# Optimization experiments

Measured on AMD Instinct MI355X. Metric: run time of the kernel, lower is better.

Reference implementation:

```python
import jax, jax.numpy as jnp
import numpy as np

N, E = 50000, 800000
IN_DIM = 128
OUT_DIM = 128
H = 8
D = OUT_DIM // H  # head_dim = 16
LN_EPS = 1e-5


def setup_inputs() -> dict:
    key = jax.random.key(0)
    ks = jax.random.split(key, 16)
    s_in = 1.0 / np.sqrt(IN_DIM)
    s_out = 1.0 / np.sqrt(OUT_DIM)
    return {
        "x": jax.random.normal(ks[0], (N, IN_DIM), dtype=jnp.float32),
        "edge_index": jax.random.randint(ks[1], (2, E), 0, N, dtype=jnp.int32),
        "edge_attr": jax.random.uniform(ks[2], (E,), dtype=jnp.float32),
        # per-head TransformerConv params, stacked over heads (heads=1 per conv)
        "Wq": jax.random.normal(ks[3], (H, IN_DIM, D), dtype=jnp.float32) * s_in,
        "bq": jnp.zeros((H, D), dtype=jnp.float32),
        "Wk": jax.random.normal(ks[4], (H, IN_DIM, D), dtype=jnp.float32) * s_in,
        "bk": jnp.zeros((H, D), dtype=jnp.float32),
        "Wv": jax.random.normal(ks[5], (H, IN_DIM, D), dtype=jnp.float32) * s_in,
        "bv": jnp.zeros((H, D), dtype=jnp.float32),
        "We": jax.random.normal(ks[6], (H, D), dtype=jnp.float32),  # lin_edge (edge_dim=1, no bias)
        "Wskip": jax.random.normal(ks[7], (H, IN_DIM, D), dtype=jnp.float32) * s_in,
        "bskip": jnp.zeros((H, D), dtype=jnp.float32),
        "Wo": jax.random.normal(ks[8], (OUT_DIM, OUT_DIM), dtype=jnp.float32) * s_out,
        "bo": jnp.zeros((OUT_DIM,), dtype=jnp.float32),
        "gamma": jnp.ones((OUT_DIM,), dtype=jnp.float32),
        "beta": jnp.zeros((OUT_DIM,), dtype=jnp.float32),
    }


def reference(x, edge_index, edge_attr, Wq, bq, Wk, bk, Wv, bv, We, Wskip, bskip, Wo, bo, gamma, beta):
    n = x.shape[0]
    h, _, d = Wq.shape
    src, dst = edge_index[0], edge_index[1]
    # node-level projections for all heads at once: [N, H, D]
    q = jnp.einsum('ni,hid->nhd', x, Wq) + bq
    k = jnp.einsum('ni,hid->nhd', x, Wk) + bk
    v = jnp.einsum('ni,hid->nhd', x, Wv) + bv
    # edge embedding: lin_edge on scalar edge_attr -> [E, H, D]
    e = edge_attr[:, None, None] * We[None, :, :]
    # attention logits per edge/head: q_dst . (k_src + e) / sqrt(d)
    ke = k[src] + e
    alpha = jnp.einsum('ehd,ehd->eh', q[dst], ke) / jnp.sqrt(jnp.asarray(d, x.dtype))
    # segment softmax over destination nodes
    m = jax.ops.segment_max(alpha, dst, num_segments=n)  # [N, H]
    m = jnp.where(jnp.isfinite(m), m, 0.0)
    ex = jnp.exp(alpha - m[dst])
    denom = jax.ops.segment_sum(ex, dst, num_segments=n)
    w = ex / jnp.maximum(denom[dst], 1e-16)  # [E, H]
    # weighted aggregation of (v_src + e)
    agg = jax.ops.segment_sum(w[:, :, None] * (v[src] + e), dst, num_segments=n)  # [N, H, D]
    # root/skip connection inside each TransformerConv
    skip = jnp.einsum('ni,hid->nhd', x, Wskip) + bskip
    heads_cat = (agg + skip).reshape(n, h * d)  # concat over heads -> [N, OUT_DIM]
    out = heads_cat @ Wo + bo
    out = out + x  # residual (in_dim == out_dim)
    mu = out.mean(-1, keepdims=True)
    var = out.var(-1, keepdims=True)
    out = (out - mu) * jax.lax.rsqrt(var + LN_EPS) * gamma + beta
    return out
```

## Files before the change

kernel.cpp:

```cpp
#include <hip/hip_runtime.h>
#include <hip/hip_bf16.h>
#include <stdint.h>
#include <math.h>

#define IN_DIM 128
#define H_HEADS 8
#define HD 16

typedef __attribute__((ext_vector_type(8))) short bf16x8;
typedef __attribute__((ext_vector_type(4))) float f32x4;

__device__ __forceinline__ unsigned short f2bf(float f) {
    __hip_bfloat16 h = __float2bfloat16(f);
    return reinterpret_cast<unsigned short&>(h);
}
__device__ __forceinline__ float bf2f(unsigned short h) {
    return __uint_as_float(((unsigned int)h) << 16);
}

__device__ __forceinline__ void split_f8(const float4 f0, const float4 f1,
                                         bf16x8& h8, bf16x8& l8) {
    float ff[8] = {f0.x, f0.y, f0.z, f0.w, f1.x, f1.y, f1.z, f1.w};
    union { bf16x8 v; unsigned short u[8]; } H, L;
#pragma unroll
    for (int j = 0; j < 8; ++j) {
        H.u[j] = f2bf(ff[j]);
        L.u[j] = f2bf(ff[j] - bf2f(H.u[j]));
    }
    h8 = H.v; l8 = L.v;
}

__device__ __forceinline__ void stage_B(const unsigned short* __restrict__ src,
                                        unsigned short* __restrict__ lds, int t)
{
#pragma unroll
    for (int j = 0; j < 8; ++j) {
        int idx16 = t + j * 256;
        int c = idx16 >> 4, kcol = idx16 & 15;
        uint4 v = *reinterpret_cast<const uint4*>(src + (size_t)c * 128 + kcol * 8);
        *reinterpret_cast<uint4*>(lds + c * 128 + ((kcol ^ (c & 15)) * 8)) = v;
    }
}
__device__ __forceinline__ bf16x8 read_B(const unsigned short* __restrict__ lds,
                                         int c, int kcol)
{
    return *reinterpret_cast<const bf16x8*>(lds + c * 128 + ((kcol ^ (c & 15)) * 8));
}

__global__ __launch_bounds__(256)
void prep_count_kernel(const float* __restrict__ Wq, const float* __restrict__ Wk,
                       const float* __restrict__ Wv, const float* __restrict__ Wsk,
                       const float* __restrict__ Wo,
                       const float* __restrict__ bq, const float* __restrict__ bk,
                       const float* __restrict__ bv, const float* __restrict__ bsk,
                       unsigned short* __restrict__ WtH, unsigned short* __restrict__ WtL,
                       float* __restrict__ bias_cat,
                       const int* __restrict__ ei, int* __restrict__ deg, int E)
{
    const int b = blockIdx.x;
    const int t = threadIdx.x;
    if (b >= 5) {
        int e = (b - 5) * 256 + t;
        if (e < E) atomicAdd(&deg[ei[E + e]], 1);
        return;
    }
    const int p = b;
    const float* src = (p == 0) ? Wq : (p == 1) ? Wk : (p == 2) ? Wv : (p == 3) ? Wsk : Wo;
    unsigned short* dh = WtH + (size_t)p * 16384;
    unsigned short* dl = WtL + (size_t)p * 16384;
#pragma unroll
    for (int j = 0; j < 64; ++j) {
        int o = t + j * 256;
        int c = o >> 7, k = o & 127;
        float v;
        if (p < 4) {
            int h = c >> 4, d = c & 15;
            v = src[(size_t)h * 2048 + (size_t)k * 16 + d];
        } else {
            v = src[(size_t)k * 128 + c];
        }
        unsigned short hi = f2bf(v);
        unsigned short lo = f2bf(v - bf2f(hi));
        dh[o] = hi; dl[o] = lo;
    }
    if (p < 4 && t < 128) {
        const float* bb = (p == 0) ? bq : (p == 1) ? bk : (p == 2) ? bv : bsk;
        bias_cat[p * 128 + t] = bb[t];
    }
}

__global__ __launch_bounds__(256)
void gemm_proj_kernel(const float* __restrict__ A,
                      const unsigned short* __restrict__ WtH_base,
                      const unsigned short* __restrict__ WtL_base,
                      const float* __restrict__ bias_cat,
                      float* __restrict__ qout, float* __restrict__ skipout,
                      unsigned short* __restrict__ kvout, int N)
{
    __shared__ unsigned short Bs[16384];
    const int t = threadIdx.x;
    const int lane = t & 63;
    const int w = t >> 6;
    const int lr = lane & 15;
    const int lk = lane >> 4;
    const int pr = blockIdx.y;
    const int brow0 = blockIdx.x * 64 + w * 16;
    const int arow = min(brow0 + lr, N - 1);
    const float* ap = A + (size_t)arow * 128;

    bf16x8 ah[4], al[4];
#pragma unroll
    for (int ks = 0; ks < 4; ++ks) {
        float4 f0 = *reinterpret_cast<const float4*>(ap + ks * 32 + lk * 8);
        float4 f1 = *reinterpret_cast<const float4*>(ap + ks * 32 + lk * 8 + 4);
        split_f8(f0, f1, ah[ks], al[ks]);
    }

    for (int pp = 0; pp < 2; ++pp) {
        const int p = pr * 2 + pp;
        f32x4 acc[8];
#pragma unroll
        for (int ni = 0; ni < 8; ++ni) acc[ni] = (f32x4){0.f, 0.f, 0.f, 0.f};

        __syncthreads();
        stage_B(WtH_base + (size_t)p * 16384, Bs, t);
        __syncthreads();
#pragma unroll
        for (int ks = 0; ks < 4; ++ks)
#pragma unroll
            for (int ni = 0; ni < 8; ++ni) {
                bf16x8 bh = read_B(Bs, ni * 16 + lr, ks * 4 + lk);
                acc[ni] = __builtin_amdgcn_mfma_f32_16x16x32_bf16(ah[ks], bh, acc[ni], 0, 0, 0);
                acc[ni] = __builtin_amdgcn_mfma_f32_16x16x32_bf16(al[ks], bh, acc[ni], 0, 0, 0);
            }
        __syncthreads();
        stage_B(WtL_base + (size_t)p * 16384, Bs, t);
        __syncthreads();
#pragma unroll
        for (int ks = 0; ks < 4; ++ks)
#pragma unroll
            for (int ni = 0; ni < 8; ++ni) {
                bf16x8 bl = read_B(Bs, ni * 16 + lr, ks * 4 + lk);
                acc[ni] = __builtin_amdgcn_mfma_f32_16x16x32_bf16(ah[ks], bl, acc[ni], 0, 0, 0);
            }

        const float* bias = bias_cat + p * 128;
        if (p == 0 || p == 3) {
            float* outp = (p == 0) ? qout : skipout;
#pragma unroll
            for (int ni = 0; ni < 8; ++ni) {
                int col = ni * 16 + lr;
                float bc = bias[col];
#pragma unroll
                for (int r = 0; r < 4; ++r) {
                    int gr = brow0 + lk * 4 + r;
                    if (gr < N) outp[(size_t)gr * 128 + col] = acc[ni][r] + bc;
                }
            }
        } else {
            unsigned int* kvu = (unsigned int*)kvout;
            const int slot = (p == 1) ? 0 : 1;
#pragma unroll
            for (int ni = 0; ni < 8; ++ni) {
                int col = ni * 16 + lr;
                float bc = bias[col];
#pragma unroll
                for (int r = 0; r < 4; ++r) {
                    unsigned int s = f2bf(acc[ni][r] + bc);
                    unsigned int o = __shfl_xor((int)s, 1);
                    int gr = brow0 + lk * 4 + r;
                    if (((lr & 1) == 0) && gr < N)
                        kvu[(size_t)gr * 128 + 2 * (col >> 1) + slot] = s | (o << 16);
                }
            }
        }
    }
}

__global__ __launch_bounds__(256)
void gemm_out_ln_kernel(const float* __restrict__ A,
                        const unsigned short* __restrict__ BtH_t,
                        const unsigned short* __restrict__ BtL_t,
                        const float* __restrict__ bo,
                        const float* __restrict__ res,
                        const float* __restrict__ gamma,
                        const float* __restrict__ beta,
                        float* __restrict__ out, int N)
{
    __shared__ unsigned short Bs[16384];
    const int t = threadIdx.x;
    const int lane = t & 63;
    const int w = t >> 6;
    const int lr = lane & 15;
    const int lk = lane >> 4;
    const int brow0 = blockIdx.x * 64 + w * 16;
    const int arow = min(brow0 + lr, N - 1);
    const float* ap = A + (size_t)arow * 128;

    bf16x8 ah[4], al[4];
#pragma unroll
    for (int ks = 0; ks < 4; ++ks) {
        float4 f0 = *reinterpret_cast<const float4*>(ap + ks * 32 + lk * 8);
        float4 f1 = *reinterpret_cast<const float4*>(ap + ks * 32 + lk * 8 + 4);
        split_f8(f0, f1, ah[ks], al[ks]);
    }

    f32x4 acc[8];
#pragma unroll
    for (int ni = 0; ni < 8; ++ni) acc[ni] = (f32x4){0.f, 0.f, 0.f, 0.f};

    stage_B(BtH_t, Bs, t);
    __syncthreads();
#pragma unroll
    for (int ks = 0; ks < 4; ++ks)
#pragma unroll
        for (int ni = 0; ni < 8; ++ni) {
            bf16x8 bh = read_B(Bs, ni * 16 + lr, ks * 4 + lk);
            acc[ni] = __builtin_amdgcn_mfma_f32_16x16x32_bf16(ah[ks], bh, acc[ni], 0, 0, 0);
            acc[ni] = __builtin_amdgcn_mfma_f32_16x16x32_bf16(al[ks], bh, acc[ni], 0, 0, 0);
        }
    __syncthreads();
    stage_B(BtL_t, Bs, t);
    __syncthreads();
#pragma unroll
    for (int ks = 0; ks < 4; ++ks)
#pragma unroll
        for (int ni = 0; ni < 8; ++ni) {
            bf16x8 bl = read_B(Bs, ni * 16 + lr, ks * 4 + lk);
            acc[ni] = __builtin_amdgcn_mfma_f32_16x16x32_bf16(ah[ks], bl, acc[ni], 0, 0, 0);
        }

#pragma unroll
    for (int ni = 0; ni < 8; ++ni) {
        int col = ni * 16 + lr;
        float bc = bo[col];
#pragma unroll
        for (int r = 0; r < 4; ++r) {
            int gr = brow0 + lk * 4 + r;
            float rv = (gr < N) ? res[(size_t)gr * 128 + col] : 0.f;
            acc[ni][r] += bc + rv;
        }
    }
#pragma unroll
    for (int r = 0; r < 4; ++r) {
        float s = 0.f, sq = 0.f;
#pragma unroll
        for (int ni = 0; ni < 8; ++ni) { float v = acc[ni][r]; s += v; sq += v * v; }
#pragma unroll
        for (int mk = 1; mk < 16; mk <<= 1) {
            s  += __shfl_xor(s, mk);
            sq += __shfl_xor(sq, mk);
        }
        float mean = s * (1.0f / 128.0f);
        float var  = sq * (1.0f / 128.0f) - mean * mean;
        float inv  = rsqrtf(var + 1e-5f);
        int gr = brow0 + lk * 4 + r;
        if (gr < N) {
#pragma unroll
            for (int ni = 0; ni < 8; ++ni) {
                int col = ni * 16 + lr;
                out[(size_t)gr * 128 + col] =
                    (acc[ni][r] - mean) * inv * gamma[col] + beta[col];
            }
        }
    }
}

__global__ __launch_bounds__(1024)
void scan_part1(const int* __restrict__ deg, int* __restrict__ offs,
                int* __restrict__ csums, int N)
{
    __shared__ int wsum[16];
    const int t = threadIdx.x;
    const int lane = t & 63, wid = t >> 6;
    const int idx = blockIdx.x * 4096 + t * 4;
    int v[4];
#pragma unroll
    for (int j = 0; j < 4; ++j) { int i = idx + j; v[j] = (i < N) ? deg[i] : 0; }
    int ls = v[0] + v[1] + v[2] + v[3];
    int inc = ls;
#pragma unroll
    for (int off = 1; off < 64; off <<= 1) {
        int y = __shfl_up(inc, off);
        if (lane >= off) inc += y;
    }
    if (lane == 63) wsum[wid] = inc;
    __syncthreads();
    if (t < 16) {
        int winc = wsum[t];
        for (int off = 1; off < 16; off <<= 1) {
            int y = __shfl_up(winc, off);
            if (t >= off) winc += y;
        }
        wsum[t] = winc;
    }
    __syncthreads();
    int wexcl = (wid == 0) ? 0 : wsum[wid - 1];
    int texcl = wexcl + (inc - ls);
    int pre = 0;
#pragma unroll
    for (int j = 0; j < 4; ++j) {
        int i = idx + j;
        if (i < N) offs[i] = texcl + pre;
        pre += v[j];
    }
    if (t == 0) csums[blockIdx.x] = wsum[15];
}

__global__ void scan_part2(int* __restrict__ csums, int nc,
                           int* __restrict__ offs, int N)
{
    const int t = threadIdx.x;
    int v = (t < nc) ? csums[t] : 0;
    int inc = v;
#pragma unroll
    for (int off = 1; off < 64; off <<= 1) {
        int y = __shfl_up(inc, off);
        if (t >= off) inc += y;
    }
    if (t < nc) csums[t] = inc - v;
    int total = __shfl(inc, nc - 1);
    if (t == 0) offs[N] = total;
}

__global__ __launch_bounds__(1024)
void scan_part3(int* __restrict__ offs, const int* __restrict__ csums,
                int* __restrict__ cursor, int N)
{
    const int coff = csums[blockIdx.x];
    const int idx = blockIdx.x * 4096 + threadIdx.x * 4;
#pragma unroll
    for (int j = 0; j < 4; ++j) {
        int i = idx + j;
        if (i < N) { int val = offs[i] + coff; offs[i] = val; cursor[i] = val; }
    }
}

__global__ void scatter_kernel(const int* __restrict__ ei, const float* __restrict__ ea,
                               int* __restrict__ cursor, int2* __restrict__ csr, int E)
{
    int e = blockIdx.x * 256 + threadIdx.x;
    if (e < E) {
        int s = ei[e], d = ei[E + e];
        int pos = atomicAdd(&cursor[d], 1);
        csr[pos] = make_int2(s, __float_as_int(ea[e]));
    }
}

__global__ __launch_bounds__(256)
void agg_kernel(const float* __restrict__ qb, const float* __restrict__ sb,
                const unsigned short* __restrict__ kvb,
                const int* __restrict__ offs, const int2* __restrict__ csr,
                const float* __restrict__ We, float* __restrict__ heads_cat, int N)
{
    const int lane = threadIdx.x & 63;
    const int node = blockIdx.x * 4 + (threadIdx.x >> 6);
    if (node >= N) return;
    const int q16  = lane & 15;
    const int quad = lane >> 4;

    const float4 qa = *reinterpret_cast<const float4*>(qb + (size_t)node * 128 + 8 * q16);
    const float4 qc = *reinterpret_cast<const float4*>(qb + (size_t)node * 128 + 8 * q16 + 4);
    const float4 wa = *reinterpret_cast<const float4*>(We + 8 * q16);
    const float4 wc = *reinterpret_cast<const float4*>(We + 8 * q16 + 4);

    float qwe = qa.x * wa.x + qa.y * wa.y + qa.z * wa.z + qa.w * wa.w
              + qc.x * wc.x + qc.y * wc.y + qc.z * wc.z + qc.w * wc.w;
    qwe += __shfl_xor(qwe, 1);

    const int e0 = offs[node];
    const int cnt = offs[node + 1] - e0;
    const int myCnt = (cnt > quad) ? ((cnt - quad + 3) >> 2) : 0;
    const int2* cp = csr + e0 + quad;
    const unsigned int* kvu = (const unsigned int*)kvb;

    float m = -__builtin_huge_valf();
    float s = 0.f, sWE = 0.f;
    float a0 = 0.f, a1 = 0.f, a2 = 0.f, a3 = 0.f;
    float a4 = 0.f, a5 = 0.f, a6 = 0.f, a7 = 0.f;

#define KVG(ec, ga, gb) do { \
    const uint4* p_ = reinterpret_cast<const uint4*>(kvu + (size_t)(ec).x * 128 + 8 * q16); \
    ga = p_[0]; gb = p_[1]; } while (0)

    int2 c0, c1, c2;
    uint4 g0a, g0b, g1a, g1b;
    if (myCnt > 0) c0 = cp[0];
    if (myCnt > 1) c1 = cp[4];
    if (myCnt > 2) c2 = cp[8];
    if (myCnt > 0) KVG(c0, g0a, g0b);
    if (myCnt > 1) KVG(c1, g1a, g1b);

    for (int j = 0; j < myCnt; ++j) {
        const float eav = __int_as_float(c0.y);
        float k0 = __uint_as_float(g0a.x << 16);
        float k1 = __uint_as_float(g0a.x & 0xffff0000u);
        float k2 = __uint_as_float(g0a.z << 16);
        float k3 = __uint_as_float(g0a.z & 0xffff0000u);
        float k4 = __uint_as_float(g0b.x << 16);
        float k5 = __uint_as_float(g0b.x & 0xffff0000u);
        float k6 = __uint_as_float(g0b.z << 16);
        float k7 = __uint_as_float(g0b.z & 0xffff0000u);
        float part = qa.x * k0 + qa.y * k1 + qa.z * k2 + qa.w * k3
                   + qc.x * k4 + qc.y * k5 + qc.z * k6 + qc.w * k7;
        part += __shfl_xor(part, 1);
        float alpha = fmaf(eav, qwe, part) * 0.25f;
        float d = alpha - m;
        if (__any(d > 8.f)) {
            float nm = fmaxf(m, alpha);
            float sc = __expf(m - nm);
            m = nm; d = alpha - m;
            s *= sc; sWE *= sc;
            a0 *= sc; a1 *= sc; a2 *= sc; a3 *= sc;
            a4 *= sc; a5 *= sc; a6 *= sc; a7 *= sc;
        }
        float pv = __expf(d);
        s += pv;
        sWE = fmaf(pv, eav, sWE);
        float v0 = __uint_as_float(g0a.y << 16);
        float v1 = __uint_as_float(g0a.y & 0xffff0000u);
        float v2 = __uint_as_float(g0a.w << 16);
        float v3 = __uint_as_float(g0a.w & 0xffff0000u);
        float v4 = __uint_as_float(g0b.y << 16);
        float v5 = __uint_as_float(g0b.y & 0xffff0000u);
        float v6 = __uint_as_float(g0b.w << 16);
        float v7 = __uint_as_float(g0b.w & 0xffff0000u);
        a0 = fmaf(pv, v0, a0); a1 = fmaf(pv, v1, a1);
        a2 = fmaf(pv, v2, a2); a3 = fmaf(pv, v3, a3);
        a4 = fmaf(pv, v4, a4); a5 = fmaf(pv, v5, a5);
        a6 = fmaf(pv, v6, a6); a7 = fmaf(pv, v7, a7);
        c0 = c1; c1 = c2;
        g0a = g1a; g0b = g1b;
        if (j + 3 < myCnt) c2 = cp[4 * j + 12];
        if (j + 2 < myCnt) KVG(c1, g1a, g1b);
    }

#pragma unroll
    for (int mk = 16; mk <= 32; mk <<= 1) {
        float om  = __shfl_xor(m, mk);
        float os  = __shfl_xor(s, mk);
        float oWE = __shfl_xor(sWE, mk);
        float o0 = __shfl_xor(a0, mk), o1 = __shfl_xor(a1, mk);
        float o2 = __shfl_xor(a2, mk), o3 = __shfl_xor(a3, mk);
        float o4 = __shfl_xor(a4, mk), o5 = __shfl_xor(a5, mk);
        float o6 = __shfl_xor(a6, mk), o7 = __shfl_xor(a7, mk);
        float nm = fmaxf(m, om);
        float eS = (s  > 0.f) ? __expf(m  - nm) : 0.f;
        float eO = (os > 0.f) ? __expf(om - nm) : 0.f;
        m = nm;
        s   = s  * eS + os  * eO;
        sWE = sWE * eS + oWE * eO;
        a0 = a0 * eS + o0 * eO; a1 = a1 * eS + o1 * eO;
        a2 = a2 * eS + o2 * eO; a3 = a3 * eS + o3 * eO;
        a4 = a4 * eS + o4 * eO; a5 = a5 * eS + o5 * eO;
        a6 = a6 * eS + o6 * eO; a7 = a7 * eS + o7 * eO;
    }

    if (quad == 0) {
        float inv = 1.0f / fmaxf(s, 1e-16f);
        const float4 s0 = *reinterpret_cast<const float4*>(sb + (size_t)node * 128 + 8 * q16);
        const float4 s1 = *reinterpret_cast<const float4*>(sb + (size_t)node * 128 + 8 * q16 + 4);
        float4 oA, oB;
        oA.x = fmaf(sWE, wa.x, a0) * inv + s0.x;
        oA.y = fmaf(sWE, wa.y, a1) * inv + s0.y;
        oA.z = fmaf(sWE, wa.z, a2) * inv + s0.z;
        oA.w = fmaf(sWE, wa.w, a3) * inv + s0.w;
        oB.x = fmaf(sWE, wc.x, a4) * inv + s1.x;
        oB.y = fmaf(sWE, wc.y, a5) * inv + s1.y;
        oB.z = fmaf(sWE, wc.z, a6) * inv + s1.z;
        oB.w = fmaf(sWE, wc.w, a7) * inv + s1.w;
        *reinterpret_cast<float4*>(heads_cat + (size_t)node * 128 + 8 * q16)     = oA;
        *reinterpret_cast<float4*>(heads_cat + (size_t)node * 128 + 8 * q16 + 4) = oB;
    }
#undef KVG
}

extern "C" void kernel_launch(void* const* d_in, const int* in_sizes, int n_in,
                              void* d_out, int out_size, void* d_ws, size_t ws_size,
                              hipStream_t stream)
{
    const float* x    = (const float*)d_in[0];
    const int*   ei   = (const int*)d_in[1];
    const float* ea   = (const float*)d_in[2];
    const float* Wq   = (const float*)d_in[3];
    const float* bq   = (const float*)d_in[4];
    const float* Wk   = (const float*)d_in[5];
    const float* bk   = (const float*)d_in[6];
    const float* Wv   = (const float*)d_in[7];
    const float* bv   = (const float*)d_in[8];
    const float* We   = (const float*)d_in[9];
    const float* Wsk  = (const float*)d_in[10];
    const float* bsk  = (const float*)d_in[11];
    const float* Wo   = (const float*)d_in[12];
    const float* bo   = (const float*)d_in[13];
    const float* gamma= (const float*)d_in[14];
    const float* beta = (const float*)d_in[15];
    const int N = in_sizes[0] / 128;
    const int E = in_sizes[1] / 2;
    float* out = (float*)d_out;

    char* w = (char*)d_ws;
    float* qarr      = (float*)w; w += (size_t)N * 128 * sizeof(float);
    float* skiparr   = (float*)w; w += (size_t)N * 128 * sizeof(float);
    unsigned short* kv = (unsigned short*)w; w += (size_t)N * 256 * sizeof(unsigned short);
    float* heads_cat = (float*)w; w += (size_t)N * 128 * sizeof(float);
    int*   deg       = (int*)w;   w += ((size_t)N + 16) * sizeof(int);
    int*   offs      = (int*)w;   w += ((size_t)N + 16) * sizeof(int);
    int*   cursor    = (int*)w;   w += ((size_t)N + 16) * sizeof(int);
    int*   csums     = (int*)w;   w += 256 * sizeof(int);
    int2*  csr       = (int2*)w;  w += (size_t)E * sizeof(int2);
    unsigned short* WtH = (unsigned short*)w; w += (size_t)5 * 16384 * sizeof(unsigned short);
    unsigned short* WtL = (unsigned short*)w; w += (size_t)5 * 16384 * sizeof(unsigned short);
    float* bias_cat  = (float*)w; w += 4 * 128 * sizeof(float);

    hipMemsetAsync(deg, 0, (size_t)N * sizeof(int), stream);

    const int cntBlocks = (E + 255) / 256;
    prep_count_kernel<<<5 + cntBlocks, 256, 0, stream>>>(Wq, Wk, Wv, Wsk, Wo, bq, bk, bv, bsk,
                                                         WtH, WtL, bias_cat, ei, deg, E);

    dim3 gProj((N + 63) / 64, 2);
    gemm_proj_kernel<<<gProj, 256, 0, stream>>>(x, WtH, WtL, bias_cat, qarr, skiparr, kv, N);

    const int nChunks = (N + 4095) / 4096;
    scan_part1<<<nChunks, 1024, 0, stream>>>(deg, offs, csums, N);
    scan_part2<<<1, 64, 0, stream>>>(csums, nChunks, offs, N);
    scan_part3<<<nChunks, 1024, 0, stream>>>(offs, csums, cursor, N);

    scatter_kernel<<<(E + 255) / 256, 256, 0, stream>>>(ei, ea, cursor, csr, E);
    agg_kernel<<<(N + 3) / 4, 256, 0, stream>>>(qarr, skiparr, kv, offs, csr, We, heads_cat, N);

    gemm_out_ln_kernel<<<(N + 63) / 64, 256, 0, stream>>>(heads_cat,
                                                          WtH + (size_t)4 * 16384,
                                                          WtL + (size_t)4 * 16384,
                                                          bo, x, gamma, beta, out, N);
}
```

Before: 327.8 us.

## Use 512-thread GEMM blocks, one projection per block, and register-prefetch weights

Both MFMA GEMM kernels now use 8 waves covering 128 rows per block. The projection kernel assigns a single weight matrix per block, with grid y of 4 instead of looping over two. The low-part weight tile is loaded into registers before the high-part compute so its global latency overlaps the MFMAs. The aim is to spread weight staging across more rows and hide load latency, at the cost of higher register pressure and reloading A once per projection.

New measurement: 337.3 us. 1.03x slower.

```diff
diff --git a/kernel.cpp b/kernel.cpp
--- a/kernel.cpp
+++ b/kernel.cpp
@@ -30,17 +30,6 @@
     h8 = H.v; l8 = L.v;
 }
 
-__device__ __forceinline__ void stage_B(const unsigned short* __restrict__ src,
-                                        unsigned short* __restrict__ lds, int t)
-{
-#pragma unroll
-    for (int j = 0; j < 8; ++j) {
-        int idx16 = t + j * 256;
-        int c = idx16 >> 4, kcol = idx16 & 15;
-        uint4 v = *reinterpret_cast<const uint4*>(src + (size_t)c * 128 + kcol * 8);
-        *reinterpret_cast<uint4*>(lds + c * 128 + ((kcol ^ (c & 15)) * 8)) = v;
-    }
-}
 __device__ __forceinline__ bf16x8 read_B(const unsigned short* __restrict__ lds,
                                          int c, int kcol)
 {
@@ -89,7 +78,7 @@
     }
 }
 
-__global__ __launch_bounds__(256)
+__global__ __launch_bounds__(512)
 void gemm_proj_kernel(const float* __restrict__ A,
                       const unsigned short* __restrict__ WtH_base,
                       const unsigned short* __restrict__ WtL_base,
@@ -103,10 +92,12 @@
     const int w = t >> 6;
     const int lr = lane & 15;
     const int lk = lane >> 4;
-    const int pr = blockIdx.y;
-    const int brow0 = blockIdx.x * 64 + w * 16;
+    const int p = blockIdx.y;
+    const int brow0 = blockIdx.x * 128 + w * 16;
     const int arow = min(brow0 + lr, N - 1);
     const float* ap = A + (size_t)arow * 128;
+    const unsigned short* BH = WtH_base + (size_t)p * 16384;
+    const unsigned short* BL = WtL_base + (size_t)p * 16384;
 
     bf16x8 ah[4], al[4];
 #pragma unroll
@@ -116,68 +107,82 @@
         split_f8(f0, f1, ah[ks], al[ks]);
     }
 
-    for (int pp = 0; pp < 2; ++pp) {
-        const int p = pr * 2 + pp;
-        f32x4 acc[8];
-#pragma unroll
-        for (int ni = 0; ni < 8; ++ni) acc[ni] = (f32x4){0.f, 0.f, 0.f, 0.f};
-
-        __syncthreads();
-        stage_B(WtH_base + (size_t)p * 16384, Bs, t);
-        __syncthreads();
-#pragma unroll
-        for (int ks = 0; ks < 4; ++ks)
-#pragma unroll
-            for (int ni = 0; ni < 8; ++ni) {
-                bf16x8 bh = read_B(Bs, ni * 16 + lr, ks * 4 + lk);
-                acc[ni] = __builtin_amdgcn_mfma_f32_16x16x32_bf16(ah[ks], bh, acc[ni], 0, 0, 0);
-                acc[ni] = __builtin_amdgcn_mfma_f32_16x16x32_bf16(al[ks], bh, acc[ni], 0, 0, 0);
+    uint4 bufH[4], bufL[4];
+#pragma unroll
+    for (int j = 0; j < 4; ++j)
+        bufH[j] = *reinterpret_cast<const uint4*>(BH + (size_t)(t + j * 512) * 8);
+#pragma unroll
+    for (int j = 0; j < 4; ++j) {
+        int idx16 = t + j * 512;
+        int c = idx16 >> 4, kcol = idx16 & 15;
+        *reinterpret_cast<uint4*>(Bs + c * 128 + ((kcol ^ (c & 15)) * 8)) = bufH[j];
+    }
+#pragma unroll
+    for (int j = 0; j < 4; ++j)
+        bufL[j] = *reinterpret_cast<const uint4*>(BL + (size_t)(t + j * 512) * 8);
+    __syncthreads();
+
+    f32x4 acc[8];
+#pragma unroll
+    for (int ni = 0; ni < 8; ++ni) acc[ni] = (f32x4){0.f, 0.f, 0.f, 0.f};
+
+#pragma unroll
+    for (int ks = 0; ks < 4; ++ks)
+#pragma unroll
+        for (int ni = 0; ni < 8; ++ni) {
+            bf16x8 bh = read_B(Bs, ni * 16 + lr, ks * 4 + lk);
+            acc[ni] = __builtin_amdgcn_mfma_f32_16x16x32_bf16(ah[ks], bh, acc[ni], 0, 0, 0);
+            acc[ni] = __builtin_amdgcn_mfma_f32_16x16x32_bf16(al[ks], bh, acc[ni], 0, 0, 0);
+        }
+    __syncthreads();
+#pragma unroll
+    for (int j = 0; j < 4; ++j) {
+        int idx16 = t + j * 512;
+        int c = idx16 >> 4, kcol = idx16 & 15;
+        *reinterpret_cast<uint4*>(Bs + c * 128 + ((kcol ^ (c & 15)) * 8)) = bufL[j];
+    }
+    __syncthreads();
+#pragma unroll
+    for (int ks = 0; ks < 4; ++ks)
+#pragma unroll
+        for (int ni = 0; ni < 8; ++ni) {
+            bf16x8 bl = read_B(Bs, ni * 16 + lr, ks * 4 + lk);
+            acc[ni] = __builtin_amdgcn_mfma_f32_16x16x32_bf16(ah[ks], bl, acc[ni], 0, 0, 0);
+        }
+
+    const float* bias = bias_cat + p * 128;
+    if (p == 0 || p == 3) {
+        float* outp = (p == 0) ? qout : skipout;
+#pragma unroll
+        for (int ni = 0; ni < 8; ++ni) {
+            int col = ni * 16 + lr;
+            float bc = bias[col];
+#pragma unroll
+            for (int r = 0; r < 4; ++r) {
+                int gr = brow0 + lk * 4 + r;
+                if (gr < N) outp[(size_t)gr * 128 + col] = acc[ni][r] + bc;
             }
-        __syncthreads();
-        stage_B(WtL_base + (size_t)p * 16384, Bs, t);
-        __syncthreads();
-#pragma unroll
-        for (int ks = 0; ks < 4; ++ks)
-#pragma unroll
-            for (int ni = 0; ni < 8; ++ni) {
-                bf16x8 bl = read_B(Bs, ni * 16 + lr, ks * 4 + lk);
-                acc[ni] = __builtin_amdgcn_mfma_f32_16x16x32_bf16(ah[ks], bl, acc[ni], 0, 0, 0);
+        }
+    } else {
+        unsigned int* kvu = (unsigned int*)kvout;
+        const int slot = (p == 1) ? 0 : 1;
+#pragma unroll
+        for (int ni = 0; ni < 8; ++ni) {
+            int col = ni * 16 + lr;
+            float bc = bias[col];
+#pragma unroll
+            for (int r = 0; r < 4; ++r) {
+                unsigned int s = f2bf(acc[ni][r] + bc);
+                unsigned int o = __shfl_xor((int)s, 1);
+                int gr = brow0 + lk * 4 + r;
+                if (((lr & 1) == 0) && gr < N)
+                    kvu[(size_t)gr * 128 + 2 * (col >> 1) + slot] = s | (o << 16);
             }
-
-        const float* bias = bias_cat + p * 128;
-        if (p == 0 || p == 3) {
-            float* outp = (p == 0) ? qout : skipout;
-#pragma unroll
-            for (int ni = 0; ni < 8; ++ni) {
-                int col = ni * 16 + lr;
-                float bc = bias[col];
-#pragma unroll
-                for (int r = 0; r < 4; ++r) {
-                    int gr = brow0 + lk * 4 + r;
-                    if (gr < N) outp[(size_t)gr * 128 + col] = acc[ni][r] + bc;
-                }
-            }
-        } else {
-            unsigned int* kvu = (unsigned int*)kvout;
-            const int slot = (p == 1) ? 0 : 1;
-#pragma unroll
-            for (int ni = 0; ni < 8; ++ni) {
-                int col = ni * 16 + lr;
-                float bc = bias[col];
-#pragma unroll
-                for (int r = 0; r < 4; ++r) {
-                    unsigned int s = f2bf(acc[ni][r] + bc);
-                    unsigned int o = __shfl_xor((int)s, 1);
-                    int gr = brow0 + lk * 4 + r;
-                    if (((lr & 1) == 0) && gr < N)
-                        kvu[(size_t)gr * 128 + 2 * (col >> 1) + slot] = s | (o << 16);
-                }
-            }
-        }
-    }
-}
-
-__global__ __launch_bounds__(256)
+        }
+    }
+}
+
+__global__ __launch_bounds__(512)
 void gemm_out_ln_kernel(const float* __restrict__ A,
                         const unsigned short* __restrict__ BtH_t,
                         const unsigned short* __restrict__ BtL_t,
@@ -193,7 +198,7 @@
     const int w = t >> 6;
     const int lr = lane & 15;
     const int lk = lane >> 4;
-    const int brow0 = blockIdx.x * 64 + w * 16;
+    const int brow0 = blockIdx.x * 128 + w * 16;
     const int arow = min(brow0 + lr, N - 1);
     const float* ap = A + (size_t)arow * 128;
 
@@ -205,12 +210,25 @@
         split_f8(f0, f1, ah[ks], al[ks]);
     }
 
+    uint4 bufH[4], bufL[4];
+#pragma unroll
+    for (int j = 0; j < 4; ++j)
+        bufH[j] = *reinterpret_cast<const uint4*>(BtH_t + (size_t)(t + j * 512) * 8);
+#pragma unroll
+    for (int j = 0; j < 4; ++j) {
+        int idx16 = t + j * 512;
+        int c = idx16 >> 4, kcol = idx16 & 15;
+        *reinterpret_cast<uint4*>(Bs + c * 128 + ((kcol ^ (c & 15)) * 8)) = bufH[j];
+    }
+#pragma unroll
+    for (int j = 0; j < 4; ++j)
+        bufL[j] = *reinterpret_cast<const uint4*>(BtL_t + (size_t)(t + j * 512) * 8);
+    __syncthreads();
+
     f32x4 acc[8];
 #pragma unroll
     for (int ni = 0; ni < 8; ++ni) acc[ni] = (f32x4){0.f, 0.f, 0.f, 0.f};
 
-    stage_B(BtH_t, Bs, t);
-    __syncthreads();
 #pragma unroll
     for (int ks = 0; ks < 4; ++ks)
 #pragma unroll
@@ -220,7 +238,12 @@
             acc[ni] = __builtin_amdgcn_mfma_f32_16x16x32_bf16(al[ks], bh, acc[ni], 0, 0, 0);
         }
     __syncthreads();
-    stage_B(BtL_t, Bs, t);
+#pragma unroll
+    for (int j = 0; j < 4; ++j) {
+        int idx16 = t + j * 512;
+        int c = idx16 >> 4, kcol = idx16 & 15;
+        *reinterpret_cast<uint4*>(Bs + c * 128 + ((kcol ^ (c & 15)) * 8)) = bufL[j];
+    }
     __syncthreads();
 #pragma unroll
     for (int ks = 0; ks < 4; ++ks)
@@ -519,8 +542,8 @@
     prep_count_kernel<<<5 + cntBlocks, 256, 0, stream>>>(Wq, Wk, Wv, Wsk, Wo, bq, bk, bv, bsk,
                                                          WtH, WtL, bias_cat, ei, deg, E);
 
-    dim3 gProj((N + 63) / 64, 2);
-    gemm_proj_kernel<<<gProj, 256, 0, stream>>>(x, WtH, WtL, bias_cat, qarr, skiparr, kv, N);
+    dim3 gProj((N + 127) / 128, 4);
+    gemm_proj_kernel<<<gProj, 512, 0, stream>>>(x, WtH, WtL, bias_cat, qarr, skiparr, kv, N);
 
     const int nChunks = (N + 4095) / 4096;
     scan_part1<<<nChunks, 1024, 0, stream>>>(deg, offs, csums, N);
@@ -530,8 +553,8 @@
     scatter_kernel<<<(E + 255) / 256, 256, 0, stream>>>(ei, ea, cursor, csr, E);
     agg_kernel<<<(N + 3) / 4, 256, 0, stream>>>(qarr, skiparr, kv, offs, csr, We, heads_cat, N);
 
-    gemm_out_ln_kernel<<<(N + 63) / 64, 256, 0, stream>>>(heads_cat,
-                                                          WtH + (size_t)4 * 16384,
-                                                          WtL + (size_t)4 * 16384,
-                                                          bo, x, gamma, beta, out, N);
-}
+    gemm_out_ln_kernel<<<(N + 127) / 128, 512, 0, stream>>>(heads_cat,
+                                                            WtH + (size_t)4 * 16384,
+                                                            WtL + (size_t)4 * 16384,
+                                                            bo, x, gamma, beta, out, N);
+}
```
